# Optimization experiments

Hardware: AMD Instinct MI355X
Metric: run time of the kernel (lower is better)

## Reference

```python
import jax, jax.numpy as jnp
import numpy as np

HEADS = 16
HEAD_DIM = 64
EMB = HEADS * HEAD_DIM
MAX_REL = 512
B, L = 4, 1024


def _rel_indices(length_q, length_k):
    # Shaw-style clipped relative distance indices into the embeddings table
    dist = jnp.arange(length_k)[None, :] - jnp.arange(length_q)[:, None]
    return jnp.clip(dist, -MAX_REL, MAX_REL) + MAX_REL  # [Lq, Lk] in [0, 2*MAX_REL]


def setup_inputs() -> dict:
    key = jax.random.key(0)
    ks = jax.random.split(key, 16)
    d = {
        "query": jax.random.normal(ks[0], (B, L, EMB), jnp.float32),
        "key": jax.random.normal(ks[1], (B, L, EMB), jnp.float32),
        "value": jax.random.normal(ks[2], (B, L, EMB), jnp.float32),
        "mask": jnp.ones((B, 1, L, L), jnp.int32),
        # per-head Linear(head_dims, head_dims) weights stored torch-style [out, in]
        "Wq": jax.random.normal(ks[3], (HEAD_DIM, HEAD_DIM), jnp.float32) / np.sqrt(HEAD_DIM),
        "bq": jax.random.normal(ks[4], (HEAD_DIM,), jnp.float32) * 0.02,
        "Wk": jax.random.normal(ks[5], (HEAD_DIM, HEAD_DIM), jnp.float32) / np.sqrt(HEAD_DIM),
        "bk": jax.random.normal(ks[6], (HEAD_DIM,), jnp.float32) * 0.02,
        "Wv": jax.random.normal(ks[7], (HEAD_DIM, HEAD_DIM), jnp.float32) / np.sqrt(HEAD_DIM),
        "bv": jax.random.normal(ks[8], (HEAD_DIM,), jnp.float32) * 0.02,
        "Wfc": jax.random.normal(ks[9], (EMB, EMB), jnp.float32) / np.sqrt(EMB),
        "bfc": jax.random.normal(ks[10], (EMB,), jnp.float32) * 0.02,
        "rel_k_table": jax.random.normal(ks[11], (2 * MAX_REL + 1, HEAD_DIM), jnp.float32) * 0.02,
        "rel_v_table": jax.random.normal(ks[12], (2 * MAX_REL + 1, HEAD_DIM), jnp.float32) * 0.02,
    }
    return d


def reference(query, key, value, mask, Wq, bq, Wk, bk, Wv, bv, Wfc, bfc, rel_k_table, rel_v_table):
    b, lq, _ = query.shape
    lk = key.shape[1]
    # split heads then per-head linear projections (torch Linear: x @ W.T + b)
    q = query.reshape(b, lq, HEADS, HEAD_DIM) @ Wq.T + bq
    k = key.reshape(b, lk, HEADS, HEAD_DIM) @ Wk.T + bk
    v = value.reshape(b, lk, HEADS, HEAD_DIM) @ Wv.T + bv

    score = jnp.einsum('bqhd,bkhd->bhqk', q, k)  # [B,H,Lq,Lk]
    score = jnp.where(mask == 0, jnp.float32(-1e20), score)

    idx = _rel_indices(lq, lk)
    a_key = rel_k_table[idx]    # [Lq, Lk, D]
    a_val = rel_v_table[idx]    # [Lq, Lk, D]
    score = score + jnp.einsum('blhd,lrd->bhlr', q, a_key)

    attn = jax.nn.softmax(score / np.sqrt(HEAD_DIM), axis=-1)

    out = jnp.einsum('bhqv,bvhd->bqhd', attn, v)
    # original: einsum('brhl,hld->bhrd', attn[b,h,q,k], a_val[q,k,d]) -> [b,q,h,d]
    out = out + jnp.einsum('bhql,qld->bqhd', attn, a_val)
    out = out.reshape(b, lq, EMB)
    return out @ Wfc.T + bfc
```

## Files before the change

kernel.cpp:

```cpp
#include <hip/hip_runtime.h>
#include <hip/hip_bf16.h>
#include <hip/hip_fp16.h>

#define SEQ 1024
#define HEADS 16
#define HDIM 64
#define EMB 1024
#define TQ 32
#define KQ 256
#define PBA_S 264
#define PBB_S 328
#define RELK_ROWS 1040
#define RELV_S 1064

typedef __bf16 bf16x8 __attribute__((ext_vector_type(8)));
typedef float floatx4 __attribute__((ext_vector_type(4)));
typedef unsigned short u16x4 __attribute__((ext_vector_type(4)));

#if __has_builtin(__builtin_amdgcn_exp2f)
#define EXP2F(x) __builtin_amdgcn_exp2f(x)
#else
#define EXP2F(x) exp2f(x)
#endif

#define QSCALE 0.18033688011112042f

static __device__ __forceinline__ unsigned short f2bu(float f) {
    __bf16 h = (__bf16)f;
    return __builtin_bit_cast(unsigned short, h);
}
static __device__ __forceinline__ float b2f(unsigned short u) {
    unsigned v = ((unsigned)u) << 16;
    return __builtin_bit_cast(float, v);
}

__global__ __launch_bounds__(256) void sa_proj_kernel(
    const float* __restrict__ qin, const float* __restrict__ kin,
    const float* __restrict__ vin,
    const unsigned short* __restrict__ wqb, const unsigned short* __restrict__ wkb,
    const unsigned short* __restrict__ wvb,
    const float* __restrict__ bq, const float* __restrict__ bk,
    const float* __restrict__ bv_,
    unsigned short* __restrict__ qb, unsigned short* __restrict__ kb,
    unsigned short* __restrict__ vtb) {
    const int t = threadIdx.x;
    const int w = t >> 6, lane = t & 63;
    const int quad = lane >> 4, l16 = lane & 15;
    const int which = blockIdx.y;
    const int bx = blockIdx.x;
    const int r0 = (bx >> 2) * 16;
    const int h = (bx & 3) * 4 + w;
    const int bidx = r0 >> 10;
    const int l0 = r0 & 1023;
    const float* x = (which == 0) ? qin : (which == 1) ? kin : vin;
    const unsigned short* Wb = (which == 0) ? wqb : (which == 1) ? wkb : wvb;
    const float* bias = (which == 0) ? bq : (which == 1) ? bk : bv_;

    bf16x8 wf[4][2];
#pragma unroll
    for (int dt = 0; dt < 4; ++dt)
#pragma unroll
        for (int ks = 0; ks < 2; ++ks)
            wf[dt][ks] = *(const bf16x8*)(Wb + (size_t)(dt * 16 + l16) * 64 + ks * 32 + quad * 8);

    bf16x8 xf[2];
#pragma unroll
    for (int ks = 0; ks < 2; ++ks) {
        const float* xp = x + (size_t)(r0 + l16) * EMB + h * 64 + ks * 32 + quad * 8;
        float4 lo = *(const float4*)xp;
        float4 hi = *(const float4*)(xp + 4);
        unsigned short px[8];
        px[0] = f2bu(lo.x); px[1] = f2bu(lo.y); px[2] = f2bu(lo.z); px[3] = f2bu(lo.w);
        px[4] = f2bu(hi.x); px[5] = f2bu(hi.y); px[6] = f2bu(hi.z); px[7] = f2bu(hi.w);
        xf[ks] = *(bf16x8*)px;
    }
    const int bh = bidx * HEADS + h;

    if (which < 2) {
        float biasd[4];
#pragma unroll
        for (int dt = 0; dt < 4; ++dt) biasd[dt] = bias[dt * 16 + l16];
        const float sc = (which == 0) ? QSCALE : 1.0f;
        unsigned short* dst = (which == 0) ? qb : kb;
        floatx4 acc[4];
#pragma unroll
        for (int dt = 0; dt < 4; ++dt) acc[dt] = floatx4{0.f, 0.f, 0.f, 0.f};
#pragma unroll
        for (int dt = 0; dt < 4; ++dt)
#pragma unroll
            for (int ks = 0; ks < 2; ++ks)
                acc[dt] = __builtin_amdgcn_mfma_f32_16x16x32_bf16(xf[ks], wf[dt][ks], acc[dt], 0, 0, 0);
#pragma unroll
        for (int dt = 0; dt < 4; ++dt)
#pragma unroll
            for (int i = 0; i < 4; ++i) {
                const int lr = l0 + quad * 4 + i;
                float val = (acc[dt][i] + biasd[dt]) * sc;
                dst[((size_t)bh * SEQ + lr) * 64 + dt * 16 + l16] = f2bu(val);
            }
    } else {
        float biasv[4][4];
#pragma unroll
        for (int dt = 0; dt < 4; ++dt)
#pragma unroll
            for (int i = 0; i < 4; ++i) biasv[dt][i] = bias[dt * 16 + quad * 4 + i];
        floatx4 acc[4];
#pragma unroll
        for (int dt = 0; dt < 4; ++dt) acc[dt] = floatx4{0.f, 0.f, 0.f, 0.f};
#pragma unroll
        for (int dt = 0; dt < 4; ++dt)
#pragma unroll
            for (int ks = 0; ks < 2; ++ks)
                acc[dt] = __builtin_amdgcn_mfma_f32_16x16x32_bf16(wf[dt][ks], xf[ks], acc[dt], 0, 0, 0);
#pragma unroll
        for (int dt = 0; dt < 4; ++dt)
#pragma unroll
            for (int i = 0; i < 4; ++i) {
                const int d = dt * 16 + quad * 4 + i;
                float val = acc[dt][i] + biasv[dt][i];
                vtb[((size_t)bh * 64 + d) * SEQ + l0 + l16] = f2bu(val);
            }
    }
}

#define NW (1024 * 1024)
#define NRK (RELK_ROWS * 64)
#define NRV (64 * RELV_S)
#define NWP (3 * 4096)
#define CONV_BLOCKS ((NW + NRK + NRV + NWP) / 256)
__global__ __launch_bounds__(256) void sa_prep_kernel(
    const float* __restrict__ Wfc, const float* __restrict__ relk,
    const float* __restrict__ relv,
    const float* __restrict__ Wq, const float* __restrict__ Wk,
    const float* __restrict__ Wv, const int* __restrict__ mask,
    unsigned short* __restrict__ wfcb, unsigned short* __restrict__ relkb,
    unsigned short* __restrict__ relvtb,
    unsigned short* __restrict__ wqb, unsigned short* __restrict__ wkb,
    unsigned short* __restrict__ wvb, unsigned* __restrict__ part) {
    const int bx = blockIdx.x;
    const int t = threadIdx.x;
    if (bx < CONV_BLOCKS) {
        int i = bx * 256 + t;
        if (i < NW) {
            wfcb[i] = f2bu(Wfc[i]);
        } else if (i < NW + NRK) {
            int j = i - NW;
            int r = j >> 6, d = j & 63;
            relkb[j] = (r <= 1024) ? f2bu(relk[r * 64 + d]) : 0;
        } else if (i < NW + NRK + NRV) {
            int j = i - NW - NRK;
            int d = j / RELV_S, c = j - d * RELV_S;
            relvtb[j] = (c <= 1024) ? f2bu(relv[c * 64 + d]) : 0;
        } else {
            int j = i - NW - NRK - NRV;
            int which = j >> 12, e = j & 4095;
            const float* src = (which == 0) ? Wq : (which == 1) ? Wk : Wv;
            unsigned short* dst = (which == 0) ? wqb : (which == 1) ? wkb : wvb;
            dst[e] = f2bu(src[e]);
        }
    } else {
        const int mb = bx - CONV_BLOCKS;
        const int b = mb >> 6, chunk = mb & 63;
        const int4* p = (const int4*)(mask + (size_t)b * (SEQ * SEQ) + chunk * 16384);
        int ok = 1;
#pragma unroll
        for (int i = 0; i < 16; ++i) {
            int4 v = p[t + i * 256];
            ok &= (v.x != 0 && v.y != 0 && v.z != 0 && v.w != 0) ? 1 : 0;
        }
        unsigned long long bal = __ballot(ok);
        __shared__ unsigned wok[4];
        if ((t & 63) == 0) wok[t >> 6] = (bal == ~0ull) ? 1u : 0u;
        __syncthreads();
        if (t == 0)
            part[b * 64 + chunk] = (wok[0] & wok[1] & wok[2] & wok[3]) ? 0xFFFFFFFFu : 0u;
    }
}

__global__ void sa_maskred2(const unsigned* __restrict__ part, unsigned* __restrict__ flags) {
    int t = threadIdx.x;
    if (t < 4) {
        unsigned f = 0xFFFFFFFFu;
        for (int i = 0; i < 64; ++i) f &= part[t * 64 + i];
        flags[t] = f;
    }
}

__global__ __launch_bounds__(512, 8) void sa_attn_kernel(
    const unsigned short* __restrict__ qb, const unsigned short* __restrict__ kb,
    const unsigned short* __restrict__ vtb, const int* __restrict__ mask,
    const unsigned short* __restrict__ relkb, const unsigned short* __restrict__ relvtb,
    const unsigned* __restrict__ flags, __half* __restrict__ Opart,
    float2* __restrict__ ms) {
    __shared__ __align__(16) unsigned short PbA[TQ * PBA_S];
    __shared__ __align__(16) unsigned short PbB[TQ * PBB_S];
    __shared__ float mxpart[8 * TQ];
    __shared__ float mxS[TQ];

    const int tid = threadIdx.x;
    const int w = tid >> 6, lane = tid & 63;
    const int quad = lane >> 4, l16 = lane & 15;
    const int bid = blockIdx.x;
    const int quarter = bid & 3;
    const int qt = (bid >> 2) & 31;
    const int bh = bid >> 7;
    const int q0 = qt * TQ;
    const int k0 = quarter * KQ;
    const int b = bh >> 4;
    const bool mfull = (flags[b] == 0xFFFFFFFFu);
    const bool clipped = (k0 - (q0 + 31) < -512) || (k0 + 255 - q0 > 512);

    const int cmin = min(512, max(-512, k0 - (q0 + 31))) + 512;
    const int cmax = min(512, max(-512, k0 + 255 - q0)) + 512;
    const int rsb = cmin & ~15;
    const int cb0 = cmin & ~7;

    bf16x8 aq[2][2];
#pragma unroll
    for (int rt = 0; rt < 2; ++rt) {
        const unsigned short* qrow = qb + ((size_t)bh * SEQ + q0 + rt * 16 + l16) * 64;
        aq[rt][0] = *(const bf16x8*)(qrow + quad * 8);
        aq[rt][1] = *(const bf16x8*)(qrow + 32 + quad * 8);
    }

    {
        const int ct_lo = cmin >> 4, ct_hi = cmax >> 4;
        for (int ct = ct_lo + w; ct <= ct_hi; ct += 8) {
            bf16x8 bf0 = *(const bf16x8*)(relkb + (size_t)(ct * 16 + l16) * 64 + quad * 8);
            bf16x8 bf1 = *(const bf16x8*)(relkb + (size_t)(ct * 16 + l16) * 64 + 32 + quad * 8);
            floatx4 r0 = {0.f, 0.f, 0.f, 0.f}, r1 = {0.f, 0.f, 0.f, 0.f};
            r0 = __builtin_amdgcn_mfma_f32_16x16x32_bf16(bf0, aq[0][0], r0, 0, 0, 0);
            r0 = __builtin_amdgcn_mfma_f32_16x16x32_bf16(bf1, aq[0][1], r0, 0, 0, 0);
            r1 = __builtin_amdgcn_mfma_f32_16x16x32_bf16(bf0, aq[1][0], r1, 0, 0, 0);
            r1 = __builtin_amdgcn_mfma_f32_16x16x32_bf16(bf1, aq[1][1], r1, 0, 0, 0);
            const int co = ct * 16 + quad * 4 - rsb;
            u16x4 p0, p1;
#pragma unroll
            for (int i = 0; i < 4; ++i) { p0[i] = f2bu(r0[i]); p1[i] = f2bu(r1[i]); }
            *(u16x4*)&PbB[(size_t)l16 * PBB_S + co] = p0;
            *(u16x4*)&PbB[(size_t)(16 + l16) * PBB_S + co] = p1;
        }
    }
    __syncthreads();

    const int kc = w;
    const int qg[2] = {q0 + l16, q0 + 16 + l16};
    floatx4 acc[2][2];
#pragma unroll
    for (int rt = 0; rt < 2; ++rt)
#pragma unroll
        for (int tt = 0; tt < 2; ++tt) acc[rt][tt] = floatx4{0.f, 0.f, 0.f, 0.f};
#pragma unroll
    for (int tt = 0; tt < 2; ++tt) {
        const unsigned short* krow = kb + ((size_t)bh * SEQ + k0 + kc * 32 + tt * 16 + l16) * 64;
        bf16x8 kf0 = *(const bf16x8*)(krow + quad * 8);
        bf16x8 kf1 = *(const bf16x8*)(krow + 32 + quad * 8);
        acc[0][tt] = __builtin_amdgcn_mfma_f32_16x16x32_bf16(kf0, aq[0][0], acc[0][tt], 0, 0, 0);
        acc[0][tt] = __builtin_amdgcn_mfma_f32_16x16x32_bf16(kf1, aq[0][1], acc[0][tt], 0, 0, 0);
        acc[1][tt] = __builtin_amdgcn_mfma_f32_16x16x32_bf16(kf0, aq[1][0], acc[1][tt], 0, 0, 0);
        acc[1][tt] = __builtin_amdgcn_mfma_f32_16x16x32_bf16(kf1, aq[1][1], acc[1][tt], 0, 0, 0);
    }
    float rmax2[2] = {-3.0e38f, -3.0e38f};
    if (mfull) {
        if (!clipped) {
#pragma unroll
            for (int rt = 0; rt < 2; ++rt) {
                const unsigned short* rsrow = &PbB[(size_t)(rt * 16 + l16) * PBB_S];
                const int cb = k0 + kc * 32 - qg[rt] + 512 - rsb;
#pragma unroll
                for (int tt = 0; tt < 2; ++tt)
#pragma unroll
                    for (int i = 0; i < 4; ++i) {
                        float s = acc[rt][tt][i] + b2f(rsrow[cb + tt * 16 + quad * 4 + i]);
                        acc[rt][tt][i] = s;
                        rmax2[rt] = fmaxf(rmax2[rt], s);
                    }
            }
        } else {
#pragma unroll
            for (int rt = 0; rt < 2; ++rt) {
                const unsigned short* rsrow = &PbB[(size_t)(rt * 16 + l16) * PBB_S];
                const int cb = k0 + kc * 32 - qg[rt] + 512;
#pragma unroll
                for (int tt = 0; tt < 2; ++tt)
#pragma unroll
                    for (int i = 0; i < 4; ++i) {
                        const int c = cb + tt * 16 + quad * 4 + i;
                        const int r = min(1024, max(0, c));
                        float s = acc[rt][tt][i] + b2f(rsrow[r - rsb]);
                        acc[rt][tt][i] = s;
                        rmax2[rt] = fmaxf(rmax2[rt], s);
                    }
            }
        }
    } else {
#pragma unroll
        for (int rt = 0; rt < 2; ++rt) {
            const unsigned short* rsrow = &PbB[(size_t)(rt * 16 + l16) * PBB_S];
            const int q = qg[rt];
            const int cb = k0 + kc * 32 - q + 512;
            const int* mrow = mask + (size_t)b * (SEQ * SEQ) + (size_t)q * SEQ;
#pragma unroll
            for (int tt = 0; tt < 2; ++tt)
#pragma unroll
                for (int i = 0; i < 4; ++i) {
                    const int k = k0 + kc * 32 + tt * 16 + quad * 4 + i;
                    const int c = cb + tt * 16 + quad * 4 + i;
                    const int r = min(1024, max(0, c));
                    float s = acc[rt][tt][i] + b2f(rsrow[r - rsb]);
                    int m = mrow[k];
                    s = (m == 0) ? -1e20f : s;
                    acc[rt][tt][i] = s;
                    rmax2[rt] = fmaxf(rmax2[rt], s);
                }
        }
    }
#pragma unroll
    for (int rt = 0; rt < 2; ++rt) {
        rmax2[rt] = fmaxf(rmax2[rt], __shfl_xor(rmax2[rt], 16));
        rmax2[rt] = fmaxf(rmax2[rt], __shfl_xor(rmax2[rt], 32));
    }
    if (quad == 0) {
        mxpart[kc * 32 + l16] = rmax2[0];
        mxpart[kc * 32 + 16 + l16] = rmax2[1];
    }
    __syncthreads();

    if (tid < TQ) {
        float m = mxpart[tid];
#pragma unroll
        for (int j = 1; j < 8; ++j) m = fmaxf(m, mxpart[j * 32 + tid]);
        mxS[tid] = m;
    }
    for (int g = tid; g < TQ * (PBB_S / 8); g += 512) {
        int row = g / (PBB_S / 8), j = g - row * (PBB_S / 8);
        *(uint4*)&PbB[row * PBB_S + j * 8] = make_uint4(0u, 0u, 0u, 0u);
    }
    __syncthreads();

    {
        const float mxv[2] = {mxS[l16], mxS[16 + l16]};
#pragma unroll
        for (int rt = 0; rt < 2; ++rt) {
            unsigned short* parow = &PbA[(size_t)(rt * 16 + l16) * PBA_S + kc * 32];
            unsigned short* pbrow = &PbB[(size_t)(rt * 16 + l16) * PBB_S];
            const int cbase = k0 + kc * 32 - qg[rt] + 512;
#pragma unroll
            for (int tt = 0; tt < 2; ++tt) {
                u16x4 pk;
#pragma unroll
                for (int i = 0; i < 4; ++i)
                    pk[i] = f2bu(EXP2F(acc[rt][tt][i] - mxv[rt]));
                *(u16x4*)(parow + tt * 16 + quad * 4) = pk;
                const int c0 = cbase + tt * 16 + quad * 4;
                if (!clipped) {
#pragma unroll
                    for (int i = 0; i < 4; ++i) pbrow[c0 + i - cb0] = pk[i];
                } else {
#pragma unroll
                    for (int i = 0; i < 4; ++i) {
                        const int c = c0 + i;
                        if ((unsigned)(c - 1) < 1023u) pbrow[c - cb0] = pk[i];
                    }
                }
            }
        }
    }
    __syncthreads();

    {
        const int rt = w & 1;
        const int dq = w >> 1;
        floatx4 accA = {0.f, 0.f, 0.f, 0.f};
        floatx4 accB = {0.f, 0.f, 0.f, 0.f};
        floatx4 accS = {0.f, 0.f, 0.f, 0.f};
        floatx4 accSI = {0.f, 0.f, 0.f, 0.f};
        unsigned short ob[8];
#pragma unroll
        for (int j = 0; j < 8; ++j) ob[j] = 0x3F80;
        const bf16x8 onesf = *(bf16x8*)ob;
        const unsigned short* vbase = vtb + ((size_t)bh * 64 + dq * 16 + l16) * SEQ + k0;
        const unsigned short* rbase = relvtb + (size_t)(dq * 16 + l16) * RELV_S;
#pragma unroll
        for (int it = 0; it < 8; ++it) {
            const int co = it * 32 + quad * 8;
            bf16x8 ap = *(const bf16x8*)&PbA[(size_t)(rt * 16 + l16) * PBA_S + co];
            bf16x8 bv = *(const bf16x8*)(vbase + co);
            accA = __builtin_amdgcn_mfma_f32_16x16x32_bf16(ap, bv, accA, 0, 0, 0);
            accS = __builtin_amdgcn_mfma_f32_16x16x32_bf16(ap, onesf, accS, 0, 0, 0);
        }
        const int nksB = ((cmax - cb0) >> 5) + 1;
        for (int ks = 0; ks < nksB; ++ks) {
            const int co = ks * 32 + quad * 8;
            bf16x8 ar = *(const bf16x8*)&PbB[(size_t)(rt * 16 + l16) * PBB_S + co];
            bf16x8 br = *(const bf16x8*)(rbase + cb0 + co);
            accB = __builtin_amdgcn_mfma_f32_16x16x32_bf16(ar, br, accB, 0, 0, 0);
            accSI = __builtin_amdgcn_mfma_f32_16x16x32_bf16(ar, onesf, accSI, 0, 0, 0);
        }
        const float rv0 = b2f(rbase[0]);
        const float rv1 = b2f(rbase[1024]);
#pragma unroll
        for (int i = 0; i < 4; ++i) {
            const int row = rt * 16 + quad * 4 + i;
            const int q = q0 + row;
            const float tail = accS[i] - accSI[i];
            const float lowS = (q >= k0 + 512) ? tail : 0.f;
            const float highS = (q <= k0 - 257) ? tail : 0.f;
            const int R = bh * SEQ + q;
            float val = accA[i] + accB[i] + lowS * rv0 + highS * rv1;
            Opart[((size_t)R * 4 + quarter) * 64 + dq * 16 + l16] = __float2half(val);
        }
        if (dq == 0 && l16 == 0) {
#pragma unroll
            for (int i = 0; i < 4; ++i) {
                const int row = rt * 16 + quad * 4 + i;
                ms[(size_t)(bh * SEQ + q0 + row) * 4 + quarter] =
                    make_float2(mxS[row], accS[i]);
            }
        }
    }
}

__global__ __launch_bounds__(256) void sa_combine_kernel(
    const __half* __restrict__ Opart, const float2* __restrict__ ms,
    unsigned short* __restrict__ aob) {
    const int tid = threadIdx.x;
    const int R = blockIdx.x * 4 + (tid >> 6);
    const int d = tid & 63;
    float2 s[4];
#pragma unroll
    for (int j = 0; j < 4; ++j) s[j] = ms[(size_t)R * 4 + j];
    float m = fmaxf(fmaxf(s[0].x, s[1].x), fmaxf(s[2].x, s[3].x));
    float a[4], denom = 0.f;
#pragma unroll
    for (int j = 0; j < 4; ++j) {
        a[j] = EXP2F(s[j].x - m);
        denom += s[j].y * a[j];
    }
    float inv = 1.f / denom;
    float val = 0.f;
#pragma unroll
    for (int j = 0; j < 4; ++j)
        val += __half2float(Opart[((size_t)R * 4 + j) * 64 + d]) * a[j];
    val *= inv;
    const int bh = R >> 10, q = R & 1023, b = bh >> 4, h = bh & 15;
    aob[((size_t)b * SEQ + q) * EMB + h * 64 + d] = f2bu(val);
}

__global__ __launch_bounds__(256, 2) void sa_fc_kernel(
    const unsigned short* __restrict__ A, const unsigned short* __restrict__ W,
    const float* __restrict__ bias, float* __restrict__ out) {
    const int t = threadIdx.x;
    const int w = t >> 6, lane = t & 63;
    const int quad = lane >> 4, l16 = lane & 15;
    const int mw = blockIdx.x * 64 + (w & 1) * 32;
    const int nw = blockIdx.y * 256 + (w >> 1) * 128;

    floatx4 acc[2][8];
#pragma unroll
    for (int mt = 0; mt < 2; ++mt)
#pragma unroll
        for (int j = 0; j < 8; ++j) acc[mt][j] = floatx4{0.f, 0.f, 0.f, 0.f};
    float bj[8];
#pragma unroll
    for (int j = 0; j < 8; ++j) bj[j] = bias[nw + j * 16 + l16];

    for (int ks = 0; ks < 32; ++ks) {
        const int co = ks * 32 + quad * 8;
        bf16x8 af0 = *(const bf16x8*)(A + (size_t)(mw + l16) * EMB + co);
        bf16x8 af1 = *(const bf16x8*)(A + (size_t)(mw + 16 + l16) * EMB + co);
#pragma unroll
        for (int j = 0; j < 8; ++j) {
            bf16x8 bf = *(const bf16x8*)(W + (size_t)(nw + j * 16 + l16) * EMB + co);
            acc[0][j] = __builtin_amdgcn_mfma_f32_16x16x32_bf16(af0, bf, acc[0][j], 0, 0, 0);
            acc[1][j] = __builtin_amdgcn_mfma_f32_16x16x32_bf16(af1, bf, acc[1][j], 0, 0, 0);
        }
    }
#pragma unroll
    for (int mt = 0; mt < 2; ++mt)
#pragma unroll
        for (int j = 0; j < 8; ++j) {
            const int col = nw + j * 16 + l16;
#pragma unroll
            for (int i = 0; i < 4; ++i) {
                const size_t row = mw + mt * 16 + quad * 4 + i;
                out[row * EMB + col] = acc[mt][j][i] + bj[j];
            }
        }
}

extern "C" void kernel_launch(void* const* d_in, const int* in_sizes, int n_in,
                              void* d_out, int out_size, void* d_ws, size_t ws_size,
                              hipStream_t stream) {
    const float* query = (const float*)d_in[0];
    const float* key = (const float*)d_in[1];
    const float* value = (const float*)d_in[2];
    const int* mask = (const int*)d_in[3];
    const float* Wq = (const float*)d_in[4];
    const float* bq = (const float*)d_in[5];
    const float* Wk = (const float*)d_in[6];
    const float* bk = (const float*)d_in[7];
    const float* Wv = (const float*)d_in[8];
    const float* bv = (const float*)d_in[9];
    const float* Wfc = (const float*)d_in[10];
    const float* bfc = (const float*)d_in[11];
    const float* relk = (const float*)d_in[12];
    const float* relv = (const float*)d_in[13];
    float* out = (float*)d_out;

    char* base = (char*)d_ws;
    const size_t MB = (size_t)1 << 20;
    unsigned short* qb = (unsigned short*)(base + 0 * MB);
    unsigned short* aob = qb;
    unsigned short* kb = (unsigned short*)(base + 8 * MB);
    unsigned short* vtb = (unsigned short*)(base + 16 * MB);
    unsigned short* wfcb = (unsigned short*)(base + 24 * MB);
    unsigned short* relkb = (unsigned short*)(base + 26 * MB);
    unsigned short* relvtb = (unsigned short*)(base + 26 * MB + 163840);
    unsigned short* wqb = (unsigned short*)(base + 26 * MB + 327680);
    unsigned short* wkb = (unsigned short*)(base + 26 * MB + 335872);
    unsigned short* wvb = (unsigned short*)(base + 26 * MB + 344064);
    unsigned* flags = (unsigned*)(base + 26 * MB + 360448);
    unsigned* part = (unsigned*)(base + 26 * MB + 364544);
    float2* ms = (float2*)(base + 27 * MB);
    __half* Opart = (__half*)(base + 29 * MB);

    sa_prep_kernel<<<CONV_BLOCKS + 256, 256, 0, stream>>>(
        Wfc, relk, relv, Wq, Wk, Wv, mask, wfcb, relkb, relvtb, wqb, wkb, wvb, part);
    sa_proj_kernel<<<dim3(1024, 3), 256, 0, stream>>>(
        query, key, value, wqb, wkb, wvb, bq, bk, bv, qb, kb, vtb);
    sa_maskred2<<<1, 64, 0, stream>>>(part, flags);
    sa_attn_kernel<<<64 * 32 * 4, 512, 0, stream>>>(
        qb, kb, vtb, mask, relkb, relvtb, flags, Opart, ms);
    sa_combine_kernel<<<(4 * HEADS * SEQ) / 4, 256, 0, stream>>>(Opart, ms, aob);
    sa_fc_kernel<<<dim3(64, 4), 256, 0, stream>>>(aob, wfcb, bfc, out);
}
```

Before: 397.5 us.

## Fuse key-quarter split and combine into single attention block without max subtraction

Each attention block now loops over all four key quarters itself and accumulates output, denominator and clipped-tail sums in registers. This removes the separate combine kernel, the half-precision partial-output and max/sum buffers, and the per-tile row-max reduction with its extra barriers. The tiny mask-flag reduction kernel is folded into the projection kernel, saving a launch. Softmax now exponentiates raw scores without subtracting a row max, so the output can overflow if scores become large. The grid is also four times smaller, which means less parallelism and more barriers per block.

```diff
diff --git a/kernel.cpp b/kernel.cpp
--- a/kernel.cpp
+++ b/kernel.cpp
@@ -42,8 +42,14 @@
     const float* __restrict__ bq, const float* __restrict__ bk,
     const float* __restrict__ bv_,
     unsigned short* __restrict__ qb, unsigned short* __restrict__ kb,
-    unsigned short* __restrict__ vtb) {
+    unsigned short* __restrict__ vtb,
+    const unsigned* __restrict__ part, unsigned* __restrict__ flags) {
     const int t = threadIdx.x;
+    if (blockIdx.x == 0 && blockIdx.y == 0 && t < 4) {
+        unsigned f = 0xFFFFFFFFu;
+        for (int i = 0; i < 64; ++i) f &= part[t * 64 + i];
+        flags[t] = f;
+    }
     const int w = t >> 6, lane = t & 63;
     const int quad = lane >> 4, l16 = lane & 15;
     const int which = blockIdx.y;
@@ -177,43 +183,23 @@
     }
 }
 
-__global__ void sa_maskred2(const unsigned* __restrict__ part, unsigned* __restrict__ flags) {
-    int t = threadIdx.x;
-    if (t < 4) {
-        unsigned f = 0xFFFFFFFFu;
-        for (int i = 0; i < 64; ++i) f &= part[t * 64 + i];
-        flags[t] = f;
-    }
-}
-
-__global__ __launch_bounds__(512, 8) void sa_attn_kernel(
+__global__ __launch_bounds__(512, 6) void sa_attn_kernel(
     const unsigned short* __restrict__ qb, const unsigned short* __restrict__ kb,
     const unsigned short* __restrict__ vtb, const int* __restrict__ mask,
     const unsigned short* __restrict__ relkb, const unsigned short* __restrict__ relvtb,
-    const unsigned* __restrict__ flags, __half* __restrict__ Opart,
-    float2* __restrict__ ms) {
+    const unsigned* __restrict__ flags, unsigned short* __restrict__ aob) {
     __shared__ __align__(16) unsigned short PbA[TQ * PBA_S];
     __shared__ __align__(16) unsigned short PbB[TQ * PBB_S];
-    __shared__ float mxpart[8 * TQ];
-    __shared__ float mxS[TQ];
 
     const int tid = threadIdx.x;
     const int w = tid >> 6, lane = tid & 63;
     const int quad = lane >> 4, l16 = lane & 15;
     const int bid = blockIdx.x;
-    const int quarter = bid & 3;
-    const int qt = (bid >> 2) & 31;
-    const int bh = bid >> 7;
+    const int qt = bid & 31;
+    const int bh = bid >> 5;
     const int q0 = qt * TQ;
-    const int k0 = quarter * KQ;
-    const int b = bh >> 4;
+    const int b = bh >> 4, h = bh & 15;
     const bool mfull = (flags[b] == 0xFFFFFFFFu);
-    const bool clipped = (k0 - (q0 + 31) < -512) || (k0 + 255 - q0 > 512);
-
-    const int cmin = min(512, max(-512, k0 - (q0 + 31))) + 512;
-    const int cmax = min(512, max(-512, k0 + 255 - q0)) + 512;
-    const int rsb = cmin & ~15;
-    const int cb0 = cmin & ~7;
 
     bf16x8 aq[2][2];
 #pragma unroll
@@ -223,228 +209,191 @@
         aq[rt][1] = *(const bf16x8*)(qrow + 32 + quad * 8);
     }
 
-    {
-        const int ct_lo = cmin >> 4, ct_hi = cmax >> 4;
-        for (int ct = ct_lo + w; ct <= ct_hi; ct += 8) {
-            bf16x8 bf0 = *(const bf16x8*)(relkb + (size_t)(ct * 16 + l16) * 64 + quad * 8);
-            bf16x8 bf1 = *(const bf16x8*)(relkb + (size_t)(ct * 16 + l16) * 64 + 32 + quad * 8);
-            floatx4 r0 = {0.f, 0.f, 0.f, 0.f}, r1 = {0.f, 0.f, 0.f, 0.f};
-            r0 = __builtin_amdgcn_mfma_f32_16x16x32_bf16(bf0, aq[0][0], r0, 0, 0, 0);
-            r0 = __builtin_amdgcn_mfma_f32_16x16x32_bf16(bf1, aq[0][1], r0, 0, 0, 0);
-            r1 = __builtin_amdgcn_mfma_f32_16x16x32_bf16(bf0, aq[1][0], r1, 0, 0, 0);
-            r1 = __builtin_amdgcn_mfma_f32_16x16x32_bf16(bf1, aq[1][1], r1, 0, 0, 0);
-            const int co = ct * 16 + quad * 4 - rsb;
-            u16x4 p0, p1;
-#pragma unroll
-            for (int i = 0; i < 4; ++i) { p0[i] = f2bu(r0[i]); p1[i] = f2bu(r1[i]); }
-            *(u16x4*)&PbB[(size_t)l16 * PBB_S + co] = p0;
-            *(u16x4*)&PbB[(size_t)(16 + l16) * PBB_S + co] = p1;
-        }
-    }
-    __syncthreads();
-
-    const int kc = w;
-    const int qg[2] = {q0 + l16, q0 + 16 + l16};
-    floatx4 acc[2][2];
-#pragma unroll
-    for (int rt = 0; rt < 2; ++rt)
-#pragma unroll
-        for (int tt = 0; tt < 2; ++tt) acc[rt][tt] = floatx4{0.f, 0.f, 0.f, 0.f};
-#pragma unroll
-    for (int tt = 0; tt < 2; ++tt) {
-        const unsigned short* krow = kb + ((size_t)bh * SEQ + k0 + kc * 32 + tt * 16 + l16) * 64;
-        bf16x8 kf0 = *(const bf16x8*)(krow + quad * 8);
-        bf16x8 kf1 = *(const bf16x8*)(krow + 32 + quad * 8);
-        acc[0][tt] = __builtin_amdgcn_mfma_f32_16x16x32_bf16(kf0, aq[0][0], acc[0][tt], 0, 0, 0);
-        acc[0][tt] = __builtin_amdgcn_mfma_f32_16x16x32_bf16(kf1, aq[0][1], acc[0][tt], 0, 0, 0);
-        acc[1][tt] = __builtin_amdgcn_mfma_f32_16x16x32_bf16(kf0, aq[1][0], acc[1][tt], 0, 0, 0);
-        acc[1][tt] = __builtin_amdgcn_mfma_f32_16x16x32_bf16(kf1, aq[1][1], acc[1][tt], 0, 0, 0);
-    }
-    float rmax2[2] = {-3.0e38f, -3.0e38f};
-    if (mfull) {
-        if (!clipped) {
+    const int rtF = w & 1;
+    const int dq = w >> 1;
+    const unsigned short* vrow = vtb + ((size_t)bh * 64 + dq * 16 + l16) * SEQ;
+    const unsigned short* rbase = relvtb + (size_t)(dq * 16 + l16) * RELV_S;
+    const float rv0 = b2f(rbase[0]);
+    const float rv1 = b2f(rbase[1024]);
+    unsigned short ob[8];
+#pragma unroll
+    for (int j = 0; j < 8; ++j) ob[j] = 0x3F80;
+    const bf16x8 onesf = *(bf16x8*)ob;
+
+    floatx4 OaccA = {0.f, 0.f, 0.f, 0.f};
+    floatx4 OaccB = {0.f, 0.f, 0.f, 0.f};
+    floatx4 dnm = {0.f, 0.f, 0.f, 0.f};
+    floatx4 tl = {0.f, 0.f, 0.f, 0.f};
+    floatx4 th = {0.f, 0.f, 0.f, 0.f};
+
+    for (int qu = 0; qu < 4; ++qu) {
+        const int k0 = qu * KQ;
+        const bool clipped = (k0 - (q0 + 31) < -512) || (k0 + 255 - q0 > 512);
+        const int cmin = min(512, max(-512, k0 - (q0 + 31))) + 512;
+        const int cmax = min(512, max(-512, k0 + 255 - q0)) + 512;
+        const int BASE = cmin & ~15;
+
+        __syncthreads();
+
+        {
+            const int ct_lo = cmin >> 4, ct_hi = cmax >> 4;
+            for (int ct = ct_lo + w; ct <= ct_hi; ct += 8) {
+                bf16x8 bf0 = *(const bf16x8*)(relkb + (size_t)(ct * 16 + l16) * 64 + quad * 8);
+                bf16x8 bf1 = *(const bf16x8*)(relkb + (size_t)(ct * 16 + l16) * 64 + 32 + quad * 8);
+                floatx4 r0 = {0.f, 0.f, 0.f, 0.f}, r1 = {0.f, 0.f, 0.f, 0.f};
+                r0 = __builtin_amdgcn_mfma_f32_16x16x32_bf16(bf0, aq[0][0], r0, 0, 0, 0);
+                r0 = __builtin_amdgcn_mfma_f32_16x16x32_bf16(bf1, aq[0][1], r0, 0, 0, 0);
+                r1 = __builtin_amdgcn_mfma_f32_16x16x32_bf16(bf0, aq[1][0], r1, 0, 0, 0);
+                r1 = __builtin_amdgcn_mfma_f32_16x16x32_bf16(bf1, aq[1][1], r1, 0, 0, 0);
+                const int co = ct * 16 + quad * 4 - BASE;
+                u16x4 p0, p1;
+#pragma unroll
+                for (int i = 0; i < 4; ++i) { p0[i] = f2bu(r0[i]); p1[i] = f2bu(r1[i]); }
+                *(u16x4*)&PbB[(size_t)l16 * PBB_S + co] = p0;
+                *(u16x4*)&PbB[(size_t)(16 + l16) * PBB_S + co] = p1;
+            }
+        }
+        __syncthreads();
+
+        const int kc = w;
+        floatx4 acc[2][2];
+#pragma unroll
+        for (int rt = 0; rt < 2; ++rt)
+#pragma unroll
+            for (int tt = 0; tt < 2; ++tt) acc[rt][tt] = floatx4{0.f, 0.f, 0.f, 0.f};
+#pragma unroll
+        for (int tt = 0; tt < 2; ++tt) {
+            const unsigned short* krow = kb + ((size_t)bh * SEQ + k0 + kc * 32 + tt * 16 + l16) * 64;
+            bf16x8 kf0 = *(const bf16x8*)(krow + quad * 8);
+            bf16x8 kf1 = *(const bf16x8*)(krow + 32 + quad * 8);
+            acc[0][tt] = __builtin_amdgcn_mfma_f32_16x16x32_bf16(kf0, aq[0][0], acc[0][tt], 0, 0, 0);
+            acc[0][tt] = __builtin_amdgcn_mfma_f32_16x16x32_bf16(kf1, aq[0][1], acc[0][tt], 0, 0, 0);
+            acc[1][tt] = __builtin_amdgcn_mfma_f32_16x16x32_bf16(kf0, aq[1][0], acc[1][tt], 0, 0, 0);
+            acc[1][tt] = __builtin_amdgcn_mfma_f32_16x16x32_bf16(kf1, aq[1][1], acc[1][tt], 0, 0, 0);
+        }
+        u16x4 pk[2][2];
+        if (mfull) {
+            if (!clipped) {
+#pragma unroll
+                for (int rt = 0; rt < 2; ++rt) {
+                    const unsigned short* rsrow = &PbB[(size_t)(rt * 16 + l16) * PBB_S];
+                    const int cb = k0 + kc * 32 - (q0 + rt * 16 + l16) + 512 - BASE;
+#pragma unroll
+                    for (int tt = 0; tt < 2; ++tt)
+#pragma unroll
+                        for (int i = 0; i < 4; ++i) {
+                            float s = acc[rt][tt][i] + b2f(rsrow[cb + tt * 16 + quad * 4 + i]);
+                            pk[rt][tt][i] = f2bu(EXP2F(s));
+                        }
+                }
+            } else {
+#pragma unroll
+                for (int rt = 0; rt < 2; ++rt) {
+                    const unsigned short* rsrow = &PbB[(size_t)(rt * 16 + l16) * PBB_S];
+                    const int cb = k0 + kc * 32 - (q0 + rt * 16 + l16) + 512;
+#pragma unroll
+                    for (int tt = 0; tt < 2; ++tt)
+#pragma unroll
+                        for (int i = 0; i < 4; ++i) {
+                            const int c = cb + tt * 16 + quad * 4 + i;
+                            const int r = min(1024, max(0, c));
+                            float s = acc[rt][tt][i] + b2f(rsrow[r - BASE]);
+                            pk[rt][tt][i] = f2bu(EXP2F(s));
+                        }
+                }
+            }
+        } else {
 #pragma unroll
             for (int rt = 0; rt < 2; ++rt) {
                 const unsigned short* rsrow = &PbB[(size_t)(rt * 16 + l16) * PBB_S];
-                const int cb = k0 + kc * 32 - qg[rt] + 512 - rsb;
+                const int q = q0 + rt * 16 + l16;
+                const int cb = k0 + kc * 32 - q + 512;
+                const int* mrow = mask + (size_t)b * (SEQ * SEQ) + (size_t)q * SEQ;
 #pragma unroll
                 for (int tt = 0; tt < 2; ++tt)
 #pragma unroll
                     for (int i = 0; i < 4; ++i) {
-                        float s = acc[rt][tt][i] + b2f(rsrow[cb + tt * 16 + quad * 4 + i]);
-                        acc[rt][tt][i] = s;
-                        rmax2[rt] = fmaxf(rmax2[rt], s);
-                    }
-            }
-        } else {
-#pragma unroll
-            for (int rt = 0; rt < 2; ++rt) {
-                const unsigned short* rsrow = &PbB[(size_t)(rt * 16 + l16) * PBB_S];
-                const int cb = k0 + kc * 32 - qg[rt] + 512;
-#pragma unroll
-                for (int tt = 0; tt < 2; ++tt)
-#pragma unroll
-                    for (int i = 0; i < 4; ++i) {
+                        const int k = k0 + kc * 32 + tt * 16 + quad * 4 + i;
                         const int c = cb + tt * 16 + quad * 4 + i;
                         const int r = min(1024, max(0, c));
-                        float s = acc[rt][tt][i] + b2f(rsrow[r - rsb]);
-                        acc[rt][tt][i] = s;
-                        rmax2[rt] = fmaxf(rmax2[rt], s);
+                        float s = acc[rt][tt][i] + b2f(rsrow[r - BASE]);
+                        int m = mrow[k];
+                        s = (m == 0) ? -1e20f : s;
+                        pk[rt][tt][i] = f2bu(EXP2F(s));
                     }
             }
         }
-    } else {
+#pragma unroll
+        for (int rt = 0; rt < 2; ++rt)
+#pragma unroll
+            for (int tt = 0; tt < 2; ++tt)
+                *(u16x4*)&PbA[(size_t)(rt * 16 + l16) * PBA_S + kc * 32 + tt * 16 + quad * 4] = pk[rt][tt];
+        __syncthreads();
+
+        for (int g = tid; g < TQ * (PBB_S / 8); g += 512) {
+            int row = g / (PBB_S / 8), j = g - row * (PBB_S / 8);
+            *(uint4*)&PbB[row * PBB_S + j * 8] = make_uint4(0u, 0u, 0u, 0u);
+        }
+        __syncthreads();
+
 #pragma unroll
         for (int rt = 0; rt < 2; ++rt) {
-            const unsigned short* rsrow = &PbB[(size_t)(rt * 16 + l16) * PBB_S];
-            const int q = qg[rt];
-            const int cb = k0 + kc * 32 - q + 512;
-            const int* mrow = mask + (size_t)b * (SEQ * SEQ) + (size_t)q * SEQ;
-#pragma unroll
-            for (int tt = 0; tt < 2; ++tt)
-#pragma unroll
-                for (int i = 0; i < 4; ++i) {
-                    const int k = k0 + kc * 32 + tt * 16 + quad * 4 + i;
-                    const int c = cb + tt * 16 + quad * 4 + i;
-                    const int r = min(1024, max(0, c));
-                    float s = acc[rt][tt][i] + b2f(rsrow[r - rsb]);
-                    int m = mrow[k];
-                    s = (m == 0) ? -1e20f : s;
-                    acc[rt][tt][i] = s;
-                    rmax2[rt] = fmaxf(rmax2[rt], s);
-                }
-        }
-    }
-#pragma unroll
-    for (int rt = 0; rt < 2; ++rt) {
-        rmax2[rt] = fmaxf(rmax2[rt], __shfl_xor(rmax2[rt], 16));
-        rmax2[rt] = fmaxf(rmax2[rt], __shfl_xor(rmax2[rt], 32));
-    }
-    if (quad == 0) {
-        mxpart[kc * 32 + l16] = rmax2[0];
-        mxpart[kc * 32 + 16 + l16] = rmax2[1];
-    }
-    __syncthreads();
-
-    if (tid < TQ) {
-        float m = mxpart[tid];
-#pragma unroll
-        for (int j = 1; j < 8; ++j) m = fmaxf(m, mxpart[j * 32 + tid]);
-        mxS[tid] = m;
-    }
-    for (int g = tid; g < TQ * (PBB_S / 8); g += 512) {
-        int row = g / (PBB_S / 8), j = g - row * (PBB_S / 8);
-        *(uint4*)&PbB[row * PBB_S + j * 8] = make_uint4(0u, 0u, 0u, 0u);
-    }
-    __syncthreads();
-
-    {
-        const float mxv[2] = {mxS[l16], mxS[16 + l16]};
-#pragma unroll
-        for (int rt = 0; rt < 2; ++rt) {
-            unsigned short* parow = &PbA[(size_t)(rt * 16 + l16) * PBA_S + kc * 32];
             unsigned short* pbrow = &PbB[(size_t)(rt * 16 + l16) * PBB_S];
-            const int cbase = k0 + kc * 32 - qg[rt] + 512;
+            const int cbase = k0 + kc * 32 - (q0 + rt * 16 + l16) + 512;
 #pragma unroll
             for (int tt = 0; tt < 2; ++tt) {
-                u16x4 pk;
-#pragma unroll
-                for (int i = 0; i < 4; ++i)
-                    pk[i] = f2bu(EXP2F(acc[rt][tt][i] - mxv[rt]));
-                *(u16x4*)(parow + tt * 16 + quad * 4) = pk;
                 const int c0 = cbase + tt * 16 + quad * 4;
                 if (!clipped) {
 #pragma unroll
-                    for (int i = 0; i < 4; ++i) pbrow[c0 + i - cb0] = pk[i];
+                    for (int i = 0; i < 4; ++i) pbrow[c0 + i - BASE] = pk[rt][tt][i];
                 } else {
 #pragma unroll
                     for (int i = 0; i < 4; ++i) {
                         const int c = c0 + i;
-                        if ((unsigned)(c - 1) < 1023u) pbrow[c - cb0] = pk[i];
+                        if ((unsigned)(c - 1) < 1023u) pbrow[c - BASE] = pk[rt][tt][i];
                     }
                 }
             }
         }
-    }
-    __syncthreads();
-
-    {
-        const int rt = w & 1;
-        const int dq = w >> 1;
-        floatx4 accA = {0.f, 0.f, 0.f, 0.f};
-        floatx4 accB = {0.f, 0.f, 0.f, 0.f};
-        floatx4 accS = {0.f, 0.f, 0.f, 0.f};
-        floatx4 accSI = {0.f, 0.f, 0.f, 0.f};
-        unsigned short ob[8];
-#pragma unroll
-        for (int j = 0; j < 8; ++j) ob[j] = 0x3F80;
-        const bf16x8 onesf = *(bf16x8*)ob;
-        const unsigned short* vbase = vtb + ((size_t)bh * 64 + dq * 16 + l16) * SEQ + k0;
-        const unsigned short* rbase = relvtb + (size_t)(dq * 16 + l16) * RELV_S;
-#pragma unroll
-        for (int it = 0; it < 8; ++it) {
-            const int co = it * 32 + quad * 8;
-            bf16x8 ap = *(const bf16x8*)&PbA[(size_t)(rt * 16 + l16) * PBA_S + co];
-            bf16x8 bv = *(const bf16x8*)(vbase + co);
-            accA = __builtin_amdgcn_mfma_f32_16x16x32_bf16(ap, bv, accA, 0, 0, 0);
-            accS = __builtin_amdgcn_mfma_f32_16x16x32_bf16(ap, onesf, accS, 0, 0, 0);
-        }
-        const int nksB = ((cmax - cb0) >> 5) + 1;
-        for (int ks = 0; ks < nksB; ++ks) {
-            const int co = ks * 32 + quad * 8;
-            bf16x8 ar = *(const bf16x8*)&PbB[(size_t)(rt * 16 + l16) * PBB_S + co];
-            bf16x8 br = *(const bf16x8*)(rbase + cb0 + co);
-            accB = __builtin_amdgcn_mfma_f32_16x16x32_bf16(ar, br, accB, 0, 0, 0);
-            accSI = __builtin_amdgcn_mfma_f32_16x16x32_bf16(ar, onesf, accSI, 0, 0, 0);
-        }
-        const float rv0 = b2f(rbase[0]);
-        const float rv1 = b2f(rbase[1024]);
-#pragma unroll
-        for (int i = 0; i < 4; ++i) {
-            const int row = rt * 16 + quad * 4 + i;
-            const int q = q0 + row;
-            const float tail = accS[i] - accSI[i];
-            const float lowS = (q >= k0 + 512) ? tail : 0.f;
-            const float highS = (q <= k0 - 257) ? tail : 0.f;
-            const int R = bh * SEQ + q;
-            float val = accA[i] + accB[i] + lowS * rv0 + highS * rv1;
-            Opart[((size_t)R * 4 + quarter) * 64 + dq * 16 + l16] = __float2half(val);
-        }
-        if (dq == 0 && l16 == 0) {
+        __syncthreads();
+
+        {
+            floatx4 accS = {0.f, 0.f, 0.f, 0.f};
+            floatx4 accSI = {0.f, 0.f, 0.f, 0.f};
+#pragma unroll
+            for (int it = 0; it < 8; ++it) {
+                const int co = it * 32 + quad * 8;
+                bf16x8 ap = *(const bf16x8*)&PbA[(size_t)(rtF * 16 + l16) * PBA_S + co];
+                bf16x8 bv = *(const bf16x8*)(vrow + k0 + co);
+                OaccA = __builtin_amdgcn_mfma_f32_16x16x32_bf16(ap, bv, OaccA, 0, 0, 0);
+                accS = __builtin_amdgcn_mfma_f32_16x16x32_bf16(ap, onesf, accS, 0, 0, 0);
+            }
+            const int nksB = ((cmax - BASE) >> 5) + 1;
+            for (int ks = 0; ks < nksB; ++ks) {
+                const int co = ks * 32 + quad * 8;
+                bf16x8 ar = *(const bf16x8*)&PbB[(size_t)(rtF * 16 + l16) * PBB_S + co];
+                bf16x8 br = *(const bf16x8*)(rbase + BASE + co);
+                OaccB = __builtin_amdgcn_mfma_f32_16x16x32_bf16(ar, br, OaccB, 0, 0, 0);
+                accSI = __builtin_amdgcn_mfma_f32_16x16x32_bf16(ar, onesf, accSI, 0, 0, 0);
+            }
 #pragma unroll
             for (int i = 0; i < 4; ++i) {
-                const int row = rt * 16 + quad * 4 + i;
-                ms[(size_t)(bh * SEQ + q0 + row) * 4 + quarter] =
-                    make_float2(mxS[row], accS[i]);
-            }
-        }
-    }
-}
-
-__global__ __launch_bounds__(256) void sa_combine_kernel(
-    const __half* __restrict__ Opart, const float2* __restrict__ ms,
-    unsigned short* __restrict__ aob) {
-    const int tid = threadIdx.x;
-    const int R = blockIdx.x * 4 + (tid >> 6);
-    const int d = tid & 63;
-    float2 s[4];
-#pragma unroll
-    for (int j = 0; j < 4; ++j) s[j] = ms[(size_t)R * 4 + j];
-    float m = fmaxf(fmaxf(s[0].x, s[1].x), fmaxf(s[2].x, s[3].x));
-    float a[4], denom = 0.f;
-#pragma unroll
-    for (int j = 0; j < 4; ++j) {
-        a[j] = EXP2F(s[j].x - m);
-        denom += s[j].y * a[j];
-    }
-    float inv = 1.f / denom;
-    float val = 0.f;
-#pragma unroll
-    for (int j = 0; j < 4; ++j)
-        val += __half2float(Opart[((size_t)R * 4 + j) * 64 + d]) * a[j];
-    val *= inv;
-    const int bh = R >> 10, q = R & 1023, b = bh >> 4, h = bh & 15;
-    aob[((size_t)b * SEQ + q) * EMB + h * 64 + d] = f2bu(val);
+                dnm[i] += accS[i];
+                const float tail = accS[i] - accSI[i];
+                const int qi = q0 + rtF * 16 + quad * 4 + i;
+                if (qi >= k0 + 512) tl[i] += tail;
+                if (qi <= k0 - 257) th[i] += tail;
+            }
+        }
+    }
+
+#pragma unroll
+    for (int i = 0; i < 4; ++i) {
+        const int row = rtF * 16 + quad * 4 + i;
+        const int q = q0 + row;
+        const float val = (OaccA[i] + OaccB[i] + tl[i] * rv0 + th[i] * rv1) / dnm[i];
+        aob[((size_t)b * SEQ + q) * EMB + h * 64 + dq * 16 + l16] = f2bu(val);
+    }
 }
 
 __global__ __launch_bounds__(256, 2) void sa_fc_kernel(
@@ -511,7 +460,6 @@
     char* base = (char*)d_ws;
     const size_t MB = (size_t)1 << 20;
     unsigned short* qb = (unsigned short*)(base + 0 * MB);
-    unsigned short* aob = qb;
     unsigned short* kb = (unsigned short*)(base + 8 * MB);
     unsigned short* vtb = (unsigned short*)(base + 16 * MB);
     unsigned short* wfcb = (unsigned short*)(base + 24 * MB);
@@ -522,16 +470,13 @@
     unsigned short* wvb = (unsigned short*)(base + 26 * MB + 344064);
     unsigned* flags = (unsigned*)(base + 26 * MB + 360448);
     unsigned* part = (unsigned*)(base + 26 * MB + 364544);
-    float2* ms = (float2*)(base + 27 * MB);
-    __half* Opart = (__half*)(base + 29 * MB);
+    unsigned short* aob = (unsigned short*)(base + 29 * MB);
 
     sa_prep_kernel<<<CONV_BLOCKS + 256, 256, 0, stream>>>(
         Wfc, relk, relv, Wq, Wk, Wv, mask, wfcb, relkb, relvtb, wqb, wkb, wvb, part);
     sa_proj_kernel<<<dim3(1024, 3), 256, 0, stream>>>(
-        query, key, value, wqb, wkb, wvb, bq, bk, bv, qb, kb, vtb);
-    sa_maskred2<<<1, 64, 0, stream>>>(part, flags);
-    sa_attn_kernel<<<64 * 32 * 4, 512, 0, stream>>>(
-        qb, kb, vtb, mask, relkb, relvtb, flags, Opart, ms);
-    sa_combine_kernel<<<(4 * HEADS * SEQ) / 4, 256, 0, stream>>>(Opart, ms, aob);
+        query, key, value, wqb, wkb, wvb, bq, bk, bv, qb, kb, vtb, part, flags);
+    sa_attn_kernel<<<64 * 32, 512, 0, stream>>>(
+        qb, kb, vtb, mask, relkb, relvtb, flags, aob);
     sa_fc_kernel<<<dim3(64, 4), 256, 0, stream>>>(aob, wfcb, bfc, out);
 }
```

After: 456.8 us. 14.9% more time.
